# Performance work log

Measured on AMD Instinct MI355X. Metric: run time of the kernel, lower is better.

The kernel has to match this reference:

```python
import jax, jax.numpy as jnp
import numpy as np

CROSS_PRUNE = 0.1  # matches init_kwargs cross_prune

N, T, D, M = 100000, 64, 128, 8


def setup_inputs() -> dict:
    key = jax.random.key(0)
    k1, k2, k3, k4 = jax.random.split(key, 4)
    x = jax.random.normal(k1, (N, D), dtype=jnp.float32)          # graph node features
    mats = jax.random.normal(k2, (M, T, D), dtype=jnp.float32) * 0.1  # cross mats (kaiming-ish scale)
    head_w = jax.random.normal(k3, (M,), dtype=jnp.float32) * 0.3     # task_head.weight [1, M] squeezed
    head_b = jax.random.normal(k4, (), dtype=jnp.float32) * 0.1       # task_head.bias
    return {"x": x, "mats": mats, "head_w": head_w, "head_b": head_b}


def reference(x, mats, head_w, head_b):
    # Original: for each mat m, cross_dot_m = mat_m @ x.T  -> M mats of [T, N];
    # then per-(i,j): task_head([cross_dot_m[i,j] for m]) = sum_m w_m * cross_dot_m[i,j] + b.
    # Linearity lets us contract the head weight into the mats first (identical math,
    # avoids materializing the [M, T, N] stack the torch code builds element-by-element).
    w_mat = jnp.einsum('m,mtd->td', head_w, mats)          # [T, D]
    cross_dot = jnp.einsum('td,nd->tn', w_mat, x) + head_b  # [T, N]
    cross_sim = jax.nn.sigmoid(cross_dot)
    # prune: entries below threshold -> 0 (dense adjacency; edge_index extraction in the
    # original is just nonzero() over this matrix, which has data-dependent shape)
    cross_adj = jnp.where(cross_sim < CROSS_PRUNE, jnp.zeros_like(cross_sim), cross_sim)
    return cross_adj
```

## Files before the change

kernel.cpp:

```cpp
#include <hip/hip_runtime.h>
#include <hip/hip_bf16.h>

#define N_NODES 100000
#define T_DIM 64
#define D_DIM 128
#define M_MATS 8
#define CROSS_PRUNE 0.1f

typedef __attribute__((ext_vector_type(8))) short bf16x8;
typedef __attribute__((ext_vector_type(4))) float f32x4;
typedef __attribute__((ext_vector_type(8))) unsigned short ushort8;

__device__ __forceinline__ void split3(float v, unsigned short& h,
                                       unsigned short& m, unsigned short& l) {
    __hip_bfloat16 bh = __float2bfloat16(v);
    float fh = __bfloat162float(bh);
    float r1 = v - fh;
    __hip_bfloat16 bm = __float2bfloat16(r1);
    float fm = __bfloat162float(bm);
    float r2 = r1 - fm;
    __hip_bfloat16 bl = __float2bfloat16(r2);
    h = __builtin_bit_cast(unsigned short, bh);
    m = __builtin_bit_cast(unsigned short, bm);
    l = __builtin_bit_cast(unsigned short, bl);
}

__global__ __launch_bounds__(256) void wmat_kernel(const float* __restrict__ mats,
                                                   const float* __restrict__ head_w,
                                                   float* __restrict__ w) {
    int i = blockIdx.x * 256 + threadIdx.x;
    if (i < T_DIM * D_DIM) {
        float acc = 0.f;
#pragma unroll
        for (int m = 0; m < M_MATS; ++m)
            acc += head_w[m] * mats[m * (T_DIM * D_DIM) + i];
        w[i] = acc;
    }
}

__global__ __launch_bounds__(256, 5) void cross_kernel(const float* __restrict__ x,
                                                       const float* __restrict__ w,
                                                       const float* __restrict__ head_b_p,
                                                       float* __restrict__ out) {
    __shared__ unsigned short xh[64 * 64];
    __shared__ unsigned short xm[64 * 64];
    __shared__ unsigned short xl[64 * 64];

    const int tid = threadIdx.x;
    const int n0 = blockIdx.x * 64;

    const int srow = tid >> 2;
    const int scol = (tid & 3) * 16;
    const int gn_s = n0 + srow;
    const float* xrow = x + (size_t)gn_s * D_DIM + scol;

    float4 p0[4], p1[4];
#pragma unroll
    for (int j = 0; j < 4; ++j) {
        p0[j] = make_float4(0.f, 0.f, 0.f, 0.f);
        p1[j] = p0[j];
        if (gn_s < N_NODES) {
            p0[j] = *reinterpret_cast<const float4*>(xrow + j * 4);
            p1[j] = *reinterpret_cast<const float4*>(xrow + 64 + j * 4);
        }
    }

#define SPLIT_STORE16(P)                                                        \
    {                                                                           \
        float fv[16];                                                           \
        _Pragma("unroll")                                                       \
        for (int j = 0; j < 4; ++j) {                                           \
            fv[j * 4 + 0] = (P)[j].x; fv[j * 4 + 1] = (P)[j].y;                 \
            fv[j * 4 + 2] = (P)[j].z; fv[j * 4 + 3] = (P)[j].w;                 \
        }                                                                       \
        _Pragma("unroll")                                                       \
        for (int u = 0; u < 2; ++u) {                                           \
            ushort8 H, M, L;                                                    \
            _Pragma("unroll")                                                   \
            for (int e = 0; e < 8; ++e) {                                       \
                unsigned short h_, m_, l_;                                      \
                split3(fv[u * 8 + e], h_, m_, l_);                              \
                H[e] = h_; M[e] = m_; L[e] = l_;                                \
            }                                                                   \
            int unit = srow * 8 + (tid & 3) * 2 + u;                            \
            int byte = (unit << 4) ^ ((srow & 7) << 4);                         \
            *reinterpret_cast<ushort8*>(reinterpret_cast<char*>(xh) + byte) = H;\
            *reinterpret_cast<ushort8*>(reinterpret_cast<char*>(xm) + byte) = M;\
            *reinterpret_cast<ushort8*>(reinterpret_cast<char*>(xl) + byte) = L;\
        }                                                                       \
    }

    SPLIT_STORE16(p0);
    __syncthreads();

    const int lane = tid & 63;
    const int tg = tid >> 6;
    const int r = lane & 15;
    const int q = lane >> 4;

    f32x4 acc[4];
#pragma unroll
    for (int nt = 0; nt < 4; ++nt) acc[nt] = (f32x4){0.f, 0.f, 0.f, 0.f};

#pragma unroll
    for (int half = 0; half < 2; ++half) {
        if (half == 1) {
            __syncthreads();
            SPLIT_STORE16(p1);
            __syncthreads();
        }

        bf16x8 ah[2], am[2], al[2];
#pragma unroll
        for (int k4 = 0; k4 < 2; ++k4) {
            const float* wp = w + (tg * 16 + r) * D_DIM + half * 64 + k4 * 32 + q * 8;
            float4 wa = *reinterpret_cast<const float4*>(wp);
            float4 wb = *reinterpret_cast<const float4*>(wp + 4);
            float wf[8] = {wa.x, wa.y, wa.z, wa.w, wb.x, wb.y, wb.z, wb.w};
#pragma unroll
            for (int j = 0; j < 8; ++j) {
                unsigned short h_, m_, l_;
                split3(wf[j], h_, m_, l_);
                ah[k4][j] = (short)h_; am[k4][j] = (short)m_; al[k4][j] = (short)l_;
            }
        }

#pragma unroll
        for (int k4 = 0; k4 < 2; ++k4) {
#pragma unroll
            for (int nt = 0; nt < 4; ++nt) {
                int byte = (((nt * 16 + r) * 64 + k4 * 32 + q * 8) << 1) ^ ((r & 7) << 4);
                bf16x8 bh = *reinterpret_cast<const bf16x8*>(
                    reinterpret_cast<const char*>(xh) + byte);
                bf16x8 bm = *reinterpret_cast<const bf16x8*>(
                    reinterpret_cast<const char*>(xm) + byte);
                bf16x8 bl = *reinterpret_cast<const bf16x8*>(
                    reinterpret_cast<const char*>(xl) + byte);
                acc[nt] = __builtin_amdgcn_mfma_f32_16x16x32_bf16(ah[k4], bh, acc[nt], 0, 0, 0);
                acc[nt] = __builtin_amdgcn_mfma_f32_16x16x32_bf16(ah[k4], bm, acc[nt], 0, 0, 0);
                acc[nt] = __builtin_amdgcn_mfma_f32_16x16x32_bf16(am[k4], bh, acc[nt], 0, 0, 0);
                acc[nt] = __builtin_amdgcn_mfma_f32_16x16x32_bf16(ah[k4], bl, acc[nt], 0, 0, 0);
                acc[nt] = __builtin_amdgcn_mfma_f32_16x16x32_bf16(al[k4], bh, acc[nt], 0, 0, 0);
                acc[nt] = __builtin_amdgcn_mfma_f32_16x16x32_bf16(am[k4], bm, acc[nt], 0, 0, 0);
            }
        }
    }

    const float hb = head_b_p[0];
#pragma unroll
    for (int nt = 0; nt < 4; ++nt) {
        int n = n0 + nt * 16 + r;
        if (n < N_NODES) {
#pragma unroll
            for (int i = 0; i < 4; ++i) {
                int t = tg * 16 + q * 4 + i;
                float v = acc[nt][i] + hb;
                float s = 1.0f / (1.0f + __expf(-v));
                if (s < CROSS_PRUNE) s = 0.0f;
                out[(size_t)t * N_NODES + n] = s;
            }
        }
    }
#undef SPLIT_STORE16
}

extern "C" void kernel_launch(void* const* d_in, const int* in_sizes, int n_in,
                              void* d_out, int out_size, void* d_ws, size_t ws_size,
                              hipStream_t stream) {
    const float* x      = (const float*)d_in[0];
    const float* mats   = (const float*)d_in[1];
    const float* head_w = (const float*)d_in[2];
    const float* head_b = (const float*)d_in[3];
    float* out = (float*)d_out;
    float* w   = (float*)d_ws;

    hipLaunchKernelGGL(wmat_kernel, dim3((T_DIM * D_DIM + 255) / 256), dim3(256), 0, stream,
                       mats, head_w, w);

    int nblk = (N_NODES + 63) / 64;
    hipLaunchKernelGGL(cross_kernel, dim3(nblk), dim3(256), 0, stream,
                       x, w, head_b, out);
}
```

Baseline: 31.99 us.

## Presplit weight into bf16 planes once and stage full-K x tile in LDS

The weight matrix is split into three bf16 planes once in the small prep kernel, not redundantly by every block, and the cross kernel loads them directly. The x tile is now staged for the full K=128 in one pass (48 KB of LDS), which drops the second split/store phase and its two barriers. MFMAs are reordered to group independent accumulators and hide latency. In exchange, occupancy falls (launch bounds 5 to 3, larger LDS), which may reduce latency hiding for the output-store-bound tail.

After: 35.16 us. 9.9% more time.

```diff
diff --git a/kernel.cpp b/kernel.cpp
--- a/kernel.cpp
+++ b/kernel.cpp
@@ -6,6 +6,7 @@
 #define D_DIM 128
 #define M_MATS 8
 #define CROSS_PRUNE 0.1f
+#define WPLANE (T_DIM * D_DIM)
 
 typedef __attribute__((ext_vector_type(8))) short bf16x8;
 typedef __attribute__((ext_vector_type(4))) float f32x4;
@@ -25,125 +26,120 @@
     l = __builtin_bit_cast(unsigned short, bl);
 }
 
-__global__ __launch_bounds__(256) void wmat_kernel(const float* __restrict__ mats,
-                                                   const float* __restrict__ head_w,
-                                                   float* __restrict__ w) {
+__global__ __launch_bounds__(256) void wsplit_kernel(const float* __restrict__ mats,
+                                                     const float* __restrict__ head_w,
+                                                     unsigned short* __restrict__ wh,
+                                                     unsigned short* __restrict__ wm,
+                                                     unsigned short* __restrict__ wl) {
     int i = blockIdx.x * 256 + threadIdx.x;
-    if (i < T_DIM * D_DIM) {
+    if (i < WPLANE) {
         float acc = 0.f;
 #pragma unroll
         for (int m = 0; m < M_MATS; ++m)
-            acc += head_w[m] * mats[m * (T_DIM * D_DIM) + i];
-        w[i] = acc;
+            acc += head_w[m] * mats[m * WPLANE + i];
+        unsigned short h, mm, l;
+        split3(acc, h, mm, l);
+        wh[i] = h; wm[i] = mm; wl[i] = l;
     }
 }
 
-__global__ __launch_bounds__(256, 5) void cross_kernel(const float* __restrict__ x,
-                                                       const float* __restrict__ w,
+__global__ __launch_bounds__(256, 3) void cross_kernel(const float* __restrict__ x,
+                                                       const unsigned short* __restrict__ wh,
+                                                       const unsigned short* __restrict__ wm,
+                                                       const unsigned short* __restrict__ wl,
                                                        const float* __restrict__ head_b_p,
                                                        float* __restrict__ out) {
-    __shared__ unsigned short xh[64 * 64];
-    __shared__ unsigned short xm[64 * 64];
-    __shared__ unsigned short xl[64 * 64];
+    __shared__ unsigned short xh[WPLANE];
+    __shared__ unsigned short xm[WPLANE];
+    __shared__ unsigned short xl[WPLANE];
 
     const int tid = threadIdx.x;
     const int n0 = blockIdx.x * 64;
-
-    const int srow = tid >> 2;
-    const int scol = (tid & 3) * 16;
-    const int gn_s = n0 + srow;
-    const float* xrow = x + (size_t)gn_s * D_DIM + scol;
-
-    float4 p0[4], p1[4];
-#pragma unroll
-    for (int j = 0; j < 4; ++j) {
-        p0[j] = make_float4(0.f, 0.f, 0.f, 0.f);
-        p1[j] = p0[j];
-        if (gn_s < N_NODES) {
-            p0[j] = *reinterpret_cast<const float4*>(xrow + j * 4);
-            p1[j] = *reinterpret_cast<const float4*>(xrow + 64 + j * 4);
-        }
-    }
-
-#define SPLIT_STORE16(P)                                                        \
-    {                                                                           \
-        float fv[16];                                                           \
-        _Pragma("unroll")                                                       \
-        for (int j = 0; j < 4; ++j) {                                           \
-            fv[j * 4 + 0] = (P)[j].x; fv[j * 4 + 1] = (P)[j].y;                 \
-            fv[j * 4 + 2] = (P)[j].z; fv[j * 4 + 3] = (P)[j].w;                 \
-        }                                                                       \
-        _Pragma("unroll")                                                       \
-        for (int u = 0; u < 2; ++u) {                                           \
-            ushort8 H, M, L;                                                    \
-            _Pragma("unroll")                                                   \
-            for (int e = 0; e < 8; ++e) {                                       \
-                unsigned short h_, m_, l_;                                      \
-                split3(fv[u * 8 + e], h_, m_, l_);                              \
-                H[e] = h_; M[e] = m_; L[e] = l_;                                \
-            }                                                                   \
-            int unit = srow * 8 + (tid & 3) * 2 + u;                            \
-            int byte = (unit << 4) ^ ((srow & 7) << 4);                         \
-            *reinterpret_cast<ushort8*>(reinterpret_cast<char*>(xh) + byte) = H;\
-            *reinterpret_cast<ushort8*>(reinterpret_cast<char*>(xm) + byte) = M;\
-            *reinterpret_cast<ushort8*>(reinterpret_cast<char*>(xl) + byte) = L;\
-        }                                                                       \
-    }
-
-    SPLIT_STORE16(p0);
-    __syncthreads();
-
     const int lane = tid & 63;
     const int tg = tid >> 6;
     const int r = lane & 15;
     const int q = lane >> 4;
+
+    const int srow = tid >> 2;
+    const int c4 = tid & 3;
+    const int gn_s = n0 + srow;
+    const float* xrow = x + (size_t)gn_s * D_DIM + c4 * 32;
+
+    float4 p[8];
+#pragma unroll
+    for (int j = 0; j < 8; ++j) {
+        p[j] = make_float4(0.f, 0.f, 0.f, 0.f);
+        if (gn_s < N_NODES)
+            p[j] = *reinterpret_cast<const float4*>(xrow + j * 4);
+    }
+
+    bf16x8 ah[4], am[4], al[4];
+#pragma unroll
+    for (int k4 = 0; k4 < 4; ++k4) {
+        int eo = (tg * 16 + r) * D_DIM + k4 * 32 + q * 8;
+        ah[k4] = *reinterpret_cast<const bf16x8*>(wh + eo);
+        am[k4] = *reinterpret_cast<const bf16x8*>(wm + eo);
+        al[k4] = *reinterpret_cast<const bf16x8*>(wl + eo);
+    }
+
+    {
+        float fv[32];
+#pragma unroll
+        for (int j = 0; j < 8; ++j) {
+            fv[j * 4 + 0] = p[j].x; fv[j * 4 + 1] = p[j].y;
+            fv[j * 4 + 2] = p[j].z; fv[j * 4 + 3] = p[j].w;
+        }
+#pragma unroll
+        for (int u = 0; u < 4; ++u) {
+            ushort8 H, M, L;
+#pragma unroll
+            for (int e = 0; e < 8; ++e) {
+                unsigned short h_, m_, l_;
+                split3(fv[u * 8 + e], h_, m_, l_);
+                H[e] = h_; M[e] = m_; L[e] = l_;
+            }
+            int unit = srow * 16 + c4 * 4 + u;
+            int byte = (unit << 4) ^ ((srow & 7) << 4);
+            *reinterpret_cast<ushort8*>(reinterpret_cast<char*>(xh) + byte) = H;
+            *reinterpret_cast<ushort8*>(reinterpret_cast<char*>(xm) + byte) = M;
+            *reinterpret_cast<ushort8*>(reinterpret_cast<char*>(xl) + byte) = L;
+        }
+    }
+    __syncthreads();
 
     f32x4 acc[4];
 #pragma unroll
     for (int nt = 0; nt < 4; ++nt) acc[nt] = (f32x4){0.f, 0.f, 0.f, 0.f};
 
 #pragma unroll
-    for (int half = 0; half < 2; ++half) {
-        if (half == 1) {
-            __syncthreads();
-            SPLIT_STORE16(p1);
-            __syncthreads();
+    for (int k4 = 0; k4 < 4; ++k4) {
+        bf16x8 bh[4], bm[4], bl[4];
+#pragma unroll
+        for (int nt = 0; nt < 4; ++nt) {
+            int eo = (nt * 16 + r) * D_DIM + k4 * 32 + q * 8;
+            int byte = (eo << 1) ^ ((r & 7) << 4);
+            bh[nt] = *reinterpret_cast<const bf16x8*>(reinterpret_cast<const char*>(xh) + byte);
+            bm[nt] = *reinterpret_cast<const bf16x8*>(reinterpret_cast<const char*>(xm) + byte);
+            bl[nt] = *reinterpret_cast<const bf16x8*>(reinterpret_cast<const char*>(xl) + byte);
         }
-
-        bf16x8 ah[2], am[2], al[2];
 #pragma unroll
-        for (int k4 = 0; k4 < 2; ++k4) {
-            const float* wp = w + (tg * 16 + r) * D_DIM + half * 64 + k4 * 32 + q * 8;
-            float4 wa = *reinterpret_cast<const float4*>(wp);
-            float4 wb = *reinterpret_cast<const float4*>(wp + 4);
-            float wf[8] = {wa.x, wa.y, wa.z, wa.w, wb.x, wb.y, wb.z, wb.w};
+        for (int nt = 0; nt < 4; ++nt)
+            acc[nt] = __builtin_amdgcn_mfma_f32_16x16x32_bf16(ah[k4], bh[nt], acc[nt], 0, 0, 0);
 #pragma unroll
-            for (int j = 0; j < 8; ++j) {
-                unsigned short h_, m_, l_;
-                split3(wf[j], h_, m_, l_);
-                ah[k4][j] = (short)h_; am[k4][j] = (short)m_; al[k4][j] = (short)l_;
-            }
-        }
-
+        for (int nt = 0; nt < 4; ++nt)
+            acc[nt] = __builtin_amdgcn_mfma_f32_16x16x32_bf16(ah[k4], bm[nt], acc[nt], 0, 0, 0);
 #pragma unroll
-        for (int k4 = 0; k4 < 2; ++k4) {
+        for (int nt = 0; nt < 4; ++nt)
+            acc[nt] = __builtin_amdgcn_mfma_f32_16x16x32_bf16(am[k4], bh[nt], acc[nt], 0, 0, 0);
 #pragma unroll
-            for (int nt = 0; nt < 4; ++nt) {
-                int byte = (((nt * 16 + r) * 64 + k4 * 32 + q * 8) << 1) ^ ((r & 7) << 4);
-                bf16x8 bh = *reinterpret_cast<const bf16x8*>(
-                    reinterpret_cast<const char*>(xh) + byte);
-                bf16x8 bm = *reinterpret_cast<const bf16x8*>(
-                    reinterpret_cast<const char*>(xm) + byte);
-                bf16x8 bl = *reinterpret_cast<const bf16x8*>(
-                    reinterpret_cast<const char*>(xl) + byte);
-                acc[nt] = __builtin_amdgcn_mfma_f32_16x16x32_bf16(ah[k4], bh, acc[nt], 0, 0, 0);
-                acc[nt] = __builtin_amdgcn_mfma_f32_16x16x32_bf16(ah[k4], bm, acc[nt], 0, 0, 0);
-                acc[nt] = __builtin_amdgcn_mfma_f32_16x16x32_bf16(am[k4], bh, acc[nt], 0, 0, 0);
-                acc[nt] = __builtin_amdgcn_mfma_f32_16x16x32_bf16(ah[k4], bl, acc[nt], 0, 0, 0);
-                acc[nt] = __builtin_amdgcn_mfma_f32_16x16x32_bf16(al[k4], bh, acc[nt], 0, 0, 0);
-                acc[nt] = __builtin_amdgcn_mfma_f32_16x16x32_bf16(am[k4], bm, acc[nt], 0, 0, 0);
-            }
-        }
+        for (int nt = 0; nt < 4; ++nt)
+            acc[nt] = __builtin_amdgcn_mfma_f32_16x16x32_bf16(ah[k4], bl[nt], acc[nt], 0, 0, 0);
+#pragma unroll
+        for (int nt = 0; nt < 4; ++nt)
+            acc[nt] = __builtin_amdgcn_mfma_f32_16x16x32_bf16(al[k4], bh[nt], acc[nt], 0, 0, 0);
+#pragma unroll
+        for (int nt = 0; nt < 4; ++nt)
+            acc[nt] = __builtin_amdgcn_mfma_f32_16x16x32_bf16(am[k4], bm[nt], acc[nt], 0, 0, 0);
     }
 
     const float hb = head_b_p[0];
@@ -161,7 +157,6 @@
             }
         }
     }
-#undef SPLIT_STORE16
 }
 
 extern "C" void kernel_launch(void* const* d_in, const int* in_sizes, int n_in,
@@ -172,12 +167,15 @@
     const float* head_w = (const float*)d_in[2];
     const float* head_b = (const float*)d_in[3];
     float* out = (float*)d_out;
-    float* w   = (float*)d_ws;
 
-    hipLaunchKernelGGL(wmat_kernel, dim3((T_DIM * D_DIM + 255) / 256), dim3(256), 0, stream,
-                       mats, head_w, w);
+    unsigned short* wh = (unsigned short*)d_ws;
+    unsigned short* wm = wh + WPLANE;
+    unsigned short* wl = wm + WPLANE;
+
+    hipLaunchKernelGGL(wsplit_kernel, dim3((WPLANE + 255) / 256), dim3(256), 0, stream,
+                       mats, head_w, wh, wm, wl);
 
     int nblk = (N_NODES + 63) / 64;
     hipLaunchKernelGGL(cross_kernel, dim3(nblk), dim3(256), 0, stream,
-                       x, w, head_b, out);
+                       x, wh, wm, wl, head_b, out);
 }
```

## Fuse head-weight contraction into cross kernel and interleave MFMA chains

Applied to the files above, without the earlier changes.

Removes the separate wmat kernel launch and instead has every block compute its slice of w = sum_m head_w[m]*mats[m] directly from mats before splitting it into bf16 pieces. The A-operand splits for all of K are now computed up front and held in registers. MFMA issue is reordered to interleave two independent accumulators so dependent chains can overlap. The trade-off is redundant per-block reads of the 8 mats (32 KB each block, mostly L2 hits), more register pressure (occupancy hint lowered from 5 to 4), and one fewer launch and sync between kernels.

Measured after the change: 72.86 us. 2.28x slower.

```diff
diff --git a/kernel.cpp b/kernel.cpp
--- a/kernel.cpp
+++ b/kernel.cpp
@@ -6,6 +6,7 @@
 #define D_DIM 128
 #define M_MATS 8
 #define CROSS_PRUNE 0.1f
+#define MSTRIDE (T_DIM * D_DIM)
 
 typedef __attribute__((ext_vector_type(8))) short bf16x8;
 typedef __attribute__((ext_vector_type(4))) float f32x4;
@@ -25,21 +26,9 @@
     l = __builtin_bit_cast(unsigned short, bl);
 }
 
-__global__ __launch_bounds__(256) void wmat_kernel(const float* __restrict__ mats,
-                                                   const float* __restrict__ head_w,
-                                                   float* __restrict__ w) {
-    int i = blockIdx.x * 256 + threadIdx.x;
-    if (i < T_DIM * D_DIM) {
-        float acc = 0.f;
-#pragma unroll
-        for (int m = 0; m < M_MATS; ++m)
-            acc += head_w[m] * mats[m * (T_DIM * D_DIM) + i];
-        w[i] = acc;
-    }
-}
-
-__global__ __launch_bounds__(256, 5) void cross_kernel(const float* __restrict__ x,
-                                                       const float* __restrict__ w,
+__global__ __launch_bounds__(256, 4) void fused_kernel(const float* __restrict__ x,
+                                                       const float* __restrict__ mats,
+                                                       const float* __restrict__ head_w,
                                                        const float* __restrict__ head_b_p,
                                                        float* __restrict__ out) {
     __shared__ unsigned short xh[64 * 64];
@@ -48,22 +37,56 @@
 
     const int tid = threadIdx.x;
     const int n0 = blockIdx.x * 64;
-
+    const int lane = tid & 63;
+    const int tg = tid >> 6;
+    const int r = lane & 15;
+    const int q = lane >> 4;
     const int srow = tid >> 2;
     const int scol = (tid & 3) * 16;
-    const int gn_s = n0 + srow;
-    const float* xrow = x + (size_t)gn_s * D_DIM + scol;
 
     float4 p0[4], p1[4];
+    {
+        const int gn = n0 + srow;
+        const float* xrow = x + (size_t)gn * D_DIM + scol;
 #pragma unroll
-    for (int j = 0; j < 4; ++j) {
-        p0[j] = make_float4(0.f, 0.f, 0.f, 0.f);
-        p1[j] = p0[j];
-        if (gn_s < N_NODES) {
-            p0[j] = *reinterpret_cast<const float4*>(xrow + j * 4);
-            p1[j] = *reinterpret_cast<const float4*>(xrow + 64 + j * 4);
+        for (int j = 0; j < 4; ++j) {
+            p0[j] = make_float4(0.f, 0.f, 0.f, 0.f);
+            p1[j] = p0[j];
+            if (gn < N_NODES) {
+                p0[j] = *reinterpret_cast<const float4*>(xrow + j * 4);
+                p1[j] = *reinterpret_cast<const float4*>(xrow + 64 + j * 4);
+            }
         }
     }
+
+    float hw[M_MATS];
+#pragma unroll
+    for (int m = 0; m < M_MATS; ++m) hw[m] = head_w[m];
+
+    bf16x8 ah[4], am[4], al[4];
+#pragma unroll
+    for (int k4 = 0; k4 < 4; ++k4) {
+        const float* wp = mats + (tg * 16 + r) * D_DIM + k4 * 32 + q * 8;
+        float wa[8];
+#pragma unroll
+        for (int e = 0; e < 8; ++e) wa[e] = 0.f;
+#pragma unroll
+        for (int m = 0; m < M_MATS; ++m) {
+            float4 v0 = *reinterpret_cast<const float4*>(wp + m * MSTRIDE);
+            float4 v1 = *reinterpret_cast<const float4*>(wp + m * MSTRIDE + 4);
+            wa[0] = fmaf(hw[m], v0.x, wa[0]); wa[1] = fmaf(hw[m], v0.y, wa[1]);
+            wa[2] = fmaf(hw[m], v0.z, wa[2]); wa[3] = fmaf(hw[m], v0.w, wa[3]);
+            wa[4] = fmaf(hw[m], v1.x, wa[4]); wa[5] = fmaf(hw[m], v1.y, wa[5]);
+            wa[6] = fmaf(hw[m], v1.z, wa[6]); wa[7] = fmaf(hw[m], v1.w, wa[7]);
+        }
+#pragma unroll
+        for (int e = 0; e < 8; ++e) {
+            unsigned short h_, m_, l_;
+            split3(wa[e], h_, m_, l_);
+            ah[k4][e] = (short)h_; am[k4][e] = (short)m_; al[k4][e] = (short)l_;
+        }
+    }
+    const float hb = head_b_p[0];
 
 #define SPLIT_STORE16(P)                                                        \
     {                                                                           \
@@ -93,11 +116,6 @@
     SPLIT_STORE16(p0);
     __syncthreads();
 
-    const int lane = tid & 63;
-    const int tg = tid >> 6;
-    const int r = lane & 15;
-    const int q = lane >> 4;
-
     f32x4 acc[4];
 #pragma unroll
     for (int nt = 0; nt < 4; ++nt) acc[nt] = (f32x4){0.f, 0.f, 0.f, 0.f};
@@ -110,43 +128,39 @@
             __syncthreads();
         }
 
-        bf16x8 ah[2], am[2], al[2];
 #pragma unroll
-        for (int k4 = 0; k4 < 2; ++k4) {
-            const float* wp = w + (tg * 16 + r) * D_DIM + half * 64 + k4 * 32 + q * 8;
-            float4 wa = *reinterpret_cast<const float4*>(wp);
-            float4 wb = *reinterpret_cast<const float4*>(wp + 4);
-            float wf[8] = {wa.x, wa.y, wa.z, wa.w, wb.x, wb.y, wb.z, wb.w};
+        for (int kk = 0; kk < 2; ++kk) {
+            const bf16x8 Ah = ah[half * 2 + kk];
+            const bf16x8 Am = am[half * 2 + kk];
+            const bf16x8 Al = al[half * 2 + kk];
 #pragma unroll
-            for (int j = 0; j < 8; ++j) {
-                unsigned short h_, m_, l_;
-                split3(wf[j], h_, m_, l_);
-                ah[k4][j] = (short)h_; am[k4][j] = (short)m_; al[k4][j] = (short)l_;
-            }
-        }
-
-#pragma unroll
-        for (int k4 = 0; k4 < 2; ++k4) {
-#pragma unroll
-            for (int nt = 0; nt < 4; ++nt) {
-                int byte = (((nt * 16 + r) * 64 + k4 * 32 + q * 8) << 1) ^ ((r & 7) << 4);
-                bf16x8 bh = *reinterpret_cast<const bf16x8*>(
-                    reinterpret_cast<const char*>(xh) + byte);
-                bf16x8 bm = *reinterpret_cast<const bf16x8*>(
-                    reinterpret_cast<const char*>(xm) + byte);
-                bf16x8 bl = *reinterpret_cast<const bf16x8*>(
-                    reinterpret_cast<const char*>(xl) + byte);
-                acc[nt] = __builtin_amdgcn_mfma_f32_16x16x32_bf16(ah[k4], bh, acc[nt], 0, 0, 0);
-                acc[nt] = __builtin_amdgcn_mfma_f32_16x16x32_bf16(ah[k4], bm, acc[nt], 0, 0, 0);
-                acc[nt] = __builtin_amdgcn_mfma_f32_16x16x32_bf16(am[k4], bh, acc[nt], 0, 0, 0);
-                acc[nt] = __builtin_amdgcn_mfma_f32_16x16x32_bf16(ah[k4], bl, acc[nt], 0, 0, 0);
-                acc[nt] = __builtin_amdgcn_mfma_f32_16x16x32_bf16(al[k4], bh, acc[nt], 0, 0, 0);
-                acc[nt] = __builtin_amdgcn_mfma_f32_16x16x32_bf16(am[k4], bm, acc[nt], 0, 0, 0);
+            for (int np = 0; np < 4; np += 2) {
+                int e0 = ((np * 16 + r) * 64 + kk * 32 + q * 8);
+                int b0 = (e0 << 1) ^ ((r & 7) << 4);
+                int e1 = (((np + 1) * 16 + r) * 64 + kk * 32 + q * 8);
+                int b1 = (e1 << 1) ^ ((r & 7) << 4);
+                bf16x8 bh0 = *reinterpret_cast<const bf16x8*>(reinterpret_cast<const char*>(xh) + b0);
+                bf16x8 bm0 = *reinterpret_cast<const bf16x8*>(reinterpret_cast<const char*>(xm) + b0);
+                bf16x8 bl0 = *reinterpret_cast<const bf16x8*>(reinterpret_cast<const char*>(xl) + b0);
+                bf16x8 bh1 = *reinterpret_cast<const bf16x8*>(reinterpret_cast<const char*>(xh) + b1);
+                bf16x8 bm1 = *reinterpret_cast<const bf16x8*>(reinterpret_cast<const char*>(xm) + b1);
+                bf16x8 bl1 = *reinterpret_cast<const bf16x8*>(reinterpret_cast<const char*>(xl) + b1);
+                acc[np]     = __builtin_amdgcn_mfma_f32_16x16x32_bf16(Ah, bh0, acc[np], 0, 0, 0);
+                acc[np + 1] = __builtin_amdgcn_mfma_f32_16x16x32_bf16(Ah, bh1, acc[np + 1], 0, 0, 0);
+                acc[np]     = __builtin_amdgcn_mfma_f32_16x16x32_bf16(Ah, bm0, acc[np], 0, 0, 0);
+                acc[np + 1] = __builtin_amdgcn_mfma_f32_16x16x32_bf16(Ah, bm1, acc[np + 1], 0, 0, 0);
+                acc[np]     = __builtin_amdgcn_mfma_f32_16x16x32_bf16(Am, bh0, acc[np], 0, 0, 0);
+                acc[np + 1] = __builtin_amdgcn_mfma_f32_16x16x32_bf16(Am, bh1, acc[np + 1], 0, 0, 0);
+                acc[np]     = __builtin_amdgcn_mfma_f32_16x16x32_bf16(Ah, bl0, acc[np], 0, 0, 0);
+                acc[np + 1] = __builtin_amdgcn_mfma_f32_16x16x32_bf16(Ah, bl1, acc[np + 1], 0, 0, 0);
+                acc[np]     = __builtin_amdgcn_mfma_f32_16x16x32_bf16(Al, bh0, acc[np], 0, 0, 0);
+                acc[np + 1] = __builtin_amdgcn_mfma_f32_16x16x32_bf16(Al, bh1, acc[np + 1], 0, 0, 0);
+                acc[np]     = __builtin_amdgcn_mfma_f32_16x16x32_bf16(Am, bm0, acc[np], 0, 0, 0);
+                acc[np + 1] = __builtin_amdgcn_mfma_f32_16x16x32_bf16(Am, bm1, acc[np + 1], 0, 0, 0);
             }
         }
     }
 
-    const float hb = head_b_p[0];
 #pragma unroll
     for (int nt = 0; nt < 4; ++nt) {
         int n = n0 + nt * 16 + r;
@@ -172,12 +186,8 @@
     const float* head_w = (const float*)d_in[2];
     const float* head_b = (const float*)d_in[3];
     float* out = (float*)d_out;
-    float* w   = (float*)d_ws;
-
-    hipLaunchKernelGGL(wmat_kernel, dim3((T_DIM * D_DIM + 255) / 256), dim3(256), 0, stream,
-                       mats, head_w, w);
 
     int nblk = (N_NODES + 63) / 64;
-    hipLaunchKernelGGL(cross_kernel, dim3(nblk), dim3(256), 0, stream,
-                       x, w, head_b, out);
+    hipLaunchKernelGGL(fused_kernel, dim3(nblk), dim3(256), 0, stream,
+                       x, mats, head_w, head_b, out);
 }
```
